# Kernel optimization log

Hardware: AMD Instinct MI355X
Metric: run time of the kernel (lower is better)

Reference implementation:

```python
import jax, jax.numpy as jnp
import numpy as np

T, C, H, S = 2048, 2048, 32, 64
H_KV = 8
L_MAA, L_DEC = 32, 64


def setup_inputs() -> dict:
    key = jax.random.key(0)
    ks = jax.random.split(key, 20)
    def n(k, shp, s=1.0):
        return jax.random.normal(k, shp, dtype=jnp.float32) * s
    sc = 0.02  # init scale for projection weights
    return dict(
        x=n(ks[0], (T, C)),
        state=jnp.zeros((1 + S, C), jnp.float32),
        new_starts=jnp.zeros((T,), bool),
        length=T,
        time_maa_x=n(ks[1], (C,), 0.1),
        time_maa_r=n(ks[2], (C,), 0.1),
        time_maa_k=n(ks[3], (C,), 0.1),
        time_maa_v=n(ks[4], (C,), 0.1),
        time_maa_w=n(ks[5], (C,), 0.1),
        time_maa_g=n(ks[6], (C,), 0.1),
        time_maa_w1=n(ks[7], (C, 5 * L_MAA), sc),
        time_maa_w2=n(ks[8], (5, L_MAA, C), sc),
        time_decay=n(ks[9], (C,), 0.5),
        time_decay_w1=n(ks[10], (C, L_DEC), sc),
        time_decay_w2=n(ks[11], (L_DEC, C), sc),
        Wq=n(ks[12], (C, H * S), sc),
        Wk=n(ks[13], (C, H_KV * S), sc),
        Wv=n(ks[14], (C, H_KV * S), sc),
        Wg=n(ks[15], (C, C), sc),
        Wo=n(ks[16], (C, C), sc),
    )


def reference(x, state, new_starts, length,
              time_maa_x, time_maa_r, time_maa_k, time_maa_v, time_maa_w, time_maa_g,
              time_maa_w1, time_maa_w2,
              time_decay, time_decay_w1, time_decay_w2,
              Wq, Wk, Wv, Wg, Wo):
    # token shift: previous token (state[0] for t=0), zeroed at sequence starts
    sx = jnp.concatenate([state[:1], x[:-1]], axis=0)
    sx = jnp.where(new_starts[:, None], 0.0, sx) - x  # [T, C]

    # data-dependent token-shift mix via LoRA (5 branches: r,k,v,w,g)
    xxx = x + sx * time_maa_x
    m = jnp.tanh(xxx @ time_maa_w1).reshape(T, 5, L_MAA).transpose(1, 0, 2)  # [5,T,L]
    m = jnp.einsum('ntl,nlc->ntc', m, time_maa_w2)  # [5,T,C]
    mr, mk, mv, mw, mg = m
    xr = x + sx * (time_maa_r + mr)
    xk = x + sx * (time_maa_k + mk)
    xv = x + sx * (time_maa_v + mv)
    xw = x + sx * (time_maa_w + mw)
    xg = x + sx * (time_maa_g + mg)

    new_state0 = x[length - 1]  # last valid token

    r = (xr @ Wq).reshape(T, H, S)
    k = (xk @ Wk).reshape(T, H_KV, S)
    v = (xv @ Wv).reshape(T, H_KV, S)

    # per-token decay via LoRA
    dec = time_decay.reshape(1, H, S) + (jnp.tanh(xw @ time_decay_w1) @ time_decay_w2).reshape(T, H, S)
    g = jax.nn.sigmoid(xg @ Wg)  # [T, C]

    reps = H // H_KV
    k = jnp.repeat(k, reps, axis=1)  # [T,H,S]
    v = jnp.repeat(v, reps, axis=1)

    log_w = jnp.maximum(-jnp.exp(dec), -5.0)  # [T,H,S]
    k = k * (1.0 - jnp.exp(log_w))

    s0 = state[1:].reshape(H, S, S)

    def step(s, inp):
        r_t, k_t, v_t, lw_t, ns_t = inp
        s = jnp.where(ns_t, 0.0, s)
        # decay along key dim, then rank-1 update k^T v
        s = s * jnp.exp(lw_t)[:, :, None] + k_t[:, :, None] * v_t[:, None, :]
        o = jnp.einsum('hk,hkv->hv', r_t, s)
        return s, o

    s_fin, out = jax.lax.scan(step, s0, (r, k, v, log_w, new_starts))

    new_state = state.at[0].set(new_state0).at[1:].set(s_fin.reshape(S, H * S))
    y = out.reshape(T, H * S) * g
    return y @ Wo, new_state
```

## Files before the change

### kernel.cpp

```cpp
#include <hip/hip_runtime.h>
#include <hip/hip_bf16.h>
#include <cmath>

#define T_DIM 2048
#define C_DIM 2048
#define NH    32
#define SS    64
#define NC    64
#define CL    32

#define SWZ(r) (((r) + ((r) >> 2)) & 3)

#define WAIT4_BARRIER() do { \
    asm volatile("s_waitcnt vmcnt(4)" ::: "memory"); \
    __builtin_amdgcn_s_barrier(); } while (0)

typedef unsigned short ushort_t;
typedef __attribute__((ext_vector_type(8))) short bf16x8;
typedef __attribute__((ext_vector_type(4))) float f32x4;

__device__ __forceinline__ ushort_t f2bf(float v) {
    union { __hip_bfloat16 b; ushort_t u; } cv;
    cv.b = __float2bfloat16(v);
    return cv.u;
}

__device__ __forceinline__ void gload_lds16(const void* g, void* l) {
    __builtin_amdgcn_global_load_lds((const __attribute__((address_space(1))) void*)g,
                                     (__attribute__((address_space(3))) void*)l,
                                     16, 0, 0);
}

__device__ __forceinline__ float bcast(float x, int k) {
    return __int_as_float(__builtin_amdgcn_readlane(__float_as_int(x), k));
}

__global__ __launch_bounds__(256)
void mega_init(const float* __restrict__ W1, const float* __restrict__ Wd1,
               const float* __restrict__ Wd2, const float* __restrict__ Wq,
               const float* __restrict__ Wk, const float* __restrict__ Wv,
               const float* __restrict__ Wg, const float* __restrict__ W2,
               ushort_t* __restrict__ W1T, ushort_t* __restrict__ Wd1T,
               ushort_t* __restrict__ Wd2T, ushort_t* __restrict__ WqT,
               ushort_t* __restrict__ WkT, ushort_t* __restrict__ WvT,
               ushort_t* __restrict__ WgT, ushort_t* __restrict__ W2Tall,
               const float* __restrict__ x, const float* __restrict__ state,
               const unsigned char* __restrict__ ns, const float* __restrict__ tmx,
               float* __restrict__ sx, ushort_t* __restrict__ xxxb,
               const int* __restrict__ len, float* __restrict__ outstate) {
    __shared__ float t[32][33];
    int bx = blockIdx.x;
    int tid = threadIdx.x;

    if (bx < 4096) {
        int i4 = bx * 256 + tid;
        int idx = i4 * 4;
        int tt = idx >> 11;
        int c = idx & 2047;
        float4 xv = *(const float4*)(x + idx);
        float4 prev;
        if (ns[tt]) prev = make_float4(0.f, 0.f, 0.f, 0.f);
        else if (tt == 0) prev = *(const float4*)(state + c);
        else prev = *(const float4*)(x + idx - C_DIM);
        float4 tm = *(const float4*)(tmx + c);
        float4 s4;
        s4.x = prev.x - xv.x;  s4.y = prev.y - xv.y;
        s4.z = prev.z - xv.z;  s4.w = prev.w - xv.w;
        *(float4*)(sx + idx) = s4;
        ushort4 xb;
        xb.x = f2bf(xv.x + s4.x * tm.x);
        xb.y = f2bf(xv.y + s4.y * tm.y);
        xb.z = f2bf(xv.z + s4.z * tm.z);
        xb.w = f2bf(xv.w + s4.w * tm.w);
        *(ushort4*)(xxxb + idx) = xb;
        return;
    }
    bx -= 4096;
    if (bx < 8) {
        int c = bx * 256 + tid;
        if (c < C_DIM)
            outstate[c] = x[(size_t)(len[0] - 1) * C_DIM + c];
        return;
    }
    bx -= 8;
    const float* W; ushort_t* WT; int K, N, nx;
    if (bx < 512)        {            W = W1;  WT = W1T;  K = 2048; N = 160;  nx = 8;  }
    else if (bx < 768)   { bx -= 512; W = Wd1; WT = Wd1T; K = 2048; N = 64;   nx = 4;  }
    else if (bx < 896)   { bx -= 768; W = Wd2; WT = Wd2T; K = 64;   N = 2048; nx = 64; }
    else if (bx < 4992)  { bx -= 896; W = Wq;  WT = WqT;  K = 2048; N = 2048; nx = 64; }
    else if (bx < 6016)  { bx -= 4992; W = Wk; WT = WkT;  K = 2048; N = 512;  nx = 16; }
    else if (bx < 7040)  { bx -= 6016; W = Wv; WT = WvT;  K = 2048; N = 512;  nx = 16; }
    else if (bx < 11136) { bx -= 7040; W = Wg; WT = WgT;  K = 2048; N = 2048; nx = 64; }
    else {
        bx -= 11136;
        int br = bx >> 6; bx &= 63;
        W = W2 + (size_t)br * 32 * C_DIM; WT = W2Tall + (size_t)br * C_DIM * 32;
        K = 32; N = 2048; nx = 64;
    }
    int n0 = (bx % nx) * 32, k0 = (bx / nx) * 32;
    int tx = tid & 31, ty = tid >> 5;
    #pragma unroll
    for (int i = 0; i < 4; ++i) {
        int k = ty + i * 8;
        float v = 0.f;
        if (n0 + tx < N) v = W[(size_t)(k0 + k) * N + n0 + tx];
        t[k][tx] = v;
    }
    __syncthreads();
    #pragma unroll
    for (int i = 0; i < 4; ++i) {
        int n = ty + i * 8;
        WT[(size_t)(n0 + n) * K + k0 + tx] = f2bf(t[tx][n]);
    }
}

__global__ __launch_bounds__(256)
void w1_splitk(const ushort_t* __restrict__ A,
               const ushort_t* __restrict__ BT,
               float* __restrict__ Wp) {
    const int lda = 2048, K = 2048;
    __shared__ ushort_t As[3][128 * 32];
    __shared__ ushort_t Bs[3][128 * 32];
    int tid = threadIdx.x;
    int wave = tid >> 6, lane = tid & 63;
    int m0 = blockIdx.y * 128, n0 = blockIdx.x * 128;
    int kbase = blockIdx.z * 256;
    float* Cf = Wp + (size_t)blockIdx.z * 2048 * 256;
    int wm = wave >> 1, wn = wave & 1;

    f32x4 acc[4][4] = {};
    int srow0 = wave * 16 + (lane >> 2);
    int schunk = lane & 3;
    int row0 = srow0, row1 = 64 + srow0;
    int gch0 = schunk ^ SWZ(row0), gch1 = schunk ^ SWZ(row1);
    const ushort_t* gA0 = A + (size_t)(m0 + row0) * lda + kbase + gch0 * 8;
    const ushort_t* gA1 = A + (size_t)(m0 + row1) * lda + kbase + gch1 * 8;
    const ushort_t* gB0 = BT + (size_t)(n0 + row0) * K + kbase + gch0 * 8;
    const ushort_t* gB1 = BT + (size_t)(n0 + row1) * K + kbase + gch1 * 8;
    int l0 = row0 * 32 + schunk * 8;
    int l1 = row1 * 32 + schunk * 8;

    const int nt = 8;
    gload_lds16(gA0, &As[0][l0]);
    gload_lds16(gB0, &Bs[0][l0]);
    gload_lds16(gA1, &As[0][l1]);
    gload_lds16(gB1, &Bs[0][l1]);
    gload_lds16(gA0 + 32, &As[1][l0]);
    gload_lds16(gB0 + 32, &Bs[1][l0]);
    gload_lds16(gA1 + 32, &As[1][l1]);
    gload_lds16(gB1 + 32, &Bs[1][l1]);
    WAIT4_BARRIER();

    int fr = lane & 15;
    int fc = lane >> 4;
    int cur = 0;
    for (int t = 0; t < nt; ++t) {
        if (t + 2 < nt) {
            int kk = (t + 2) << 5;
            int nb = cur == 0 ? 2 : cur - 1;
            gload_lds16(gA0 + kk, &As[nb][l0]);
            gload_lds16(gB0 + kk, &Bs[nb][l0]);
            gload_lds16(gA1 + kk, &As[nb][l1]);
            gload_lds16(gB1 + kk, &Bs[nb][l1]);
        }
        bf16x8 af[4], bfr[4];
        #pragma unroll
        for (int mi = 0; mi < 4; ++mi) {
            int r = wm * 64 + mi * 16 + fr;
            af[mi] = *(const bf16x8*)(&As[cur][r * 32 + ((fc ^ SWZ(r)) * 8)]);
        }
        #pragma unroll
        for (int ni = 0; ni < 4; ++ni) {
            int c = wn * 64 + ni * 16 + fr;
            bfr[ni] = *(const bf16x8*)(&Bs[cur][c * 32 + ((fc ^ SWZ(c)) * 8)]);
        }
        #pragma unroll
        for (int mi = 0; mi < 4; ++mi)
            #pragma unroll
            for (int ni = 0; ni < 4; ++ni)
                acc[mi][ni] = __builtin_amdgcn_mfma_f32_16x16x32_bf16(
                    af[mi], bfr[ni], acc[mi][ni], 0, 0, 0);
        WAIT4_BARRIER();
        cur = cur == 2 ? 0 : cur + 1;
    }

    int colin = lane & 15;
    int rquad = lane >> 4;
    #pragma unroll
    for (int mi = 0; mi < 4; ++mi)
        #pragma unroll
        for (int reg = 0; reg < 4; ++reg) {
            int row = m0 + wm * 64 + mi * 16 + rquad * 4 + reg;
            #pragma unroll
            for (int ni = 0; ni < 4; ++ni) {
                int col = n0 + wn * 64 + ni * 16 + colin;
                Cf[(size_t)row * 256 + col] = acc[mi][ni][reg];
            }
        }
}

__global__ __launch_bounds__(256)
void w1_reduce(const float* __restrict__ Wp, ushort_t* __restrict__ mtlb) {
    int idx = (blockIdx.x * 256 + threadIdx.x) * 4;
    float4 s = *(const float4*)(Wp + idx);
    #pragma unroll
    for (int z = 1; z < 8; ++z) {
        float4 p = *(const float4*)(Wp + (size_t)z * 2048 * 256 + idx);
        s.x += p.x; s.y += p.y; s.z += p.z; s.w += p.w;
    }
    ushort4 o;
    o.x = f2bf(tanhf(s.x)); o.y = f2bf(tanhf(s.y));
    o.z = f2bf(tanhf(s.z)); o.w = f2bf(tanhf(s.w));
    *(ushort4*)(mtlb + idx) = o;
}

__global__ __launch_bounds__(256)
void gemm_wo(const ushort_t* __restrict__ A, const ushort_t* __restrict__ BT,
             float* __restrict__ Cf) {
    const int lda = 2048, K = 2048, ldc = 2048;
    __shared__ ushort_t As[3][128 * 32];
    __shared__ ushort_t Bs[3][128 * 32];
    int tid = threadIdx.x;
    int wave = tid >> 6, lane = tid & 63;
    int id = blockIdx.y * 16 + blockIdx.x;
    int xcd = id & 7, j = id >> 3;
    int m0 = ((xcd >> 1) * 4 + (j & 3)) * 128;
    int n0 = ((xcd & 1) * 8 + (j >> 2)) * 128;
    int wm = wave >> 1, wn = wave & 1;

    f32x4 acc[4][4] = {};
    int srow0 = wave * 16 + (lane >> 2);
    int schunk = lane & 3;
    int row0 = srow0, row1 = 64 + srow0;
    int gch0 = schunk ^ SWZ(row0), gch1 = schunk ^ SWZ(row1);
    const ushort_t* gA0 = A + (size_t)(m0 + row0) * lda + gch0 * 8;
    const ushort_t* gA1 = A + (size_t)(m0 + row1) * lda + gch1 * 8;
    const ushort_t* gB0 = BT + (size_t)(n0 + row0) * K + gch0 * 8;
    const ushort_t* gB1 = BT + (size_t)(n0 + row1) * K + gch1 * 8;
    int l0 = row0 * 32 + schunk * 8;
    int l1 = row1 * 32 + schunk * 8;

    const int nt = K >> 5;
    gload_lds16(gA0, &As[0][l0]);
    gload_lds16(gB0, &Bs[0][l0]);
    gload_lds16(gA1, &As[0][l1]);
    gload_lds16(gB1, &Bs[0][l1]);
    gload_lds16(gA0 + 32, &As[1][l0]);
    gload_lds16(gB0 + 32, &Bs[1][l0]);
    gload_lds16(gA1 + 32, &As[1][l1]);
    gload_lds16(gB1 + 32, &Bs[1][l1]);
    WAIT4_BARRIER();

    int fr = lane & 15;
    int fc = lane >> 4;
    int cur = 0;
    for (int t = 0; t < nt; ++t) {
        if (t + 2 < nt) {
            int kk = (t + 2) << 5;
            int nb = cur == 0 ? 2 : cur - 1;
            gload_lds16(gA0 + kk, &As[nb][l0]);
            gload_lds16(gB0 + kk, &Bs[nb][l0]);
            gload_lds16(gA1 + kk, &As[nb][l1]);
            gload_lds16(gB1 + kk, &Bs[nb][l1]);
        }
        bf16x8 af[4], bfr[4];
        #pragma unroll
        for (int mi = 0; mi < 4; ++mi) {
            int r = wm * 64 + mi * 16 + fr;
            af[mi] = *(const bf16x8*)(&As[cur][r * 32 + ((fc ^ SWZ(r)) * 8)]);
        }
        #pragma unroll
        for (int ni = 0; ni < 4; ++ni) {
            int c = wn * 64 + ni * 16 + fr;
            bfr[ni] = *(const bf16x8*)(&Bs[cur][c * 32 + ((fc ^ SWZ(c)) * 8)]);
        }
        #pragma unroll
        for (int mi = 0; mi < 4; ++mi)
            #pragma unroll
            for (int ni = 0; ni < 4; ++ni)
                acc[mi][ni] = __builtin_amdgcn_mfma_f32_16x16x32_bf16(
                    af[mi], bfr[ni], acc[mi][ni], 0, 0, 0);
        WAIT4_BARRIER();
        cur = cur == 2 ? 0 : cur + 1;
    }

    int colin = lane & 15;
    int rquad = lane >> 4;
    #pragma unroll
    for (int mi = 0; mi < 4; ++mi)
        #pragma unroll
        for (int reg = 0; reg < 4; ++reg) {
            int row = m0 + wm * 64 + mi * 16 + rquad * 4 + reg;
            #pragma unroll
            for (int ni = 0; ni < 4; ++ni) {
                int col = n0 + wn * 64 + ni * 16 + colin;
                Cf[(size_t)row * ldc + col] = acc[mi][ni][reg];
            }
        }
}

__global__ __launch_bounds__(256)
void gemm_fused5(const ushort_t* __restrict__ xw, const ushort_t* __restrict__ xk,
                 const ushort_t* __restrict__ xv, const ushort_t* __restrict__ xr,
                 const ushort_t* __restrict__ xg,
                 const ushort_t* __restrict__ Wd1T, const ushort_t* __restrict__ WkT,
                 const ushort_t* __restrict__ WvT, const ushort_t* __restrict__ WqT,
                 const ushort_t* __restrict__ WgT,
                 ushort_t* __restrict__ tw, float* __restrict__ k0g,
                 float* __restrict__ v0g, float* __restrict__ rg,
                 float* __restrict__ gg) {
    const int K = 2048, lda = 2048;
    int id = blockIdx.y * 41 + blockIdx.x;
    int swz = (id & 7) * 82 + (id >> 3);
    int bx = swz >> 4;
    int m0 = (swz & 15) * 128;

    const ushort_t* A; const ushort_t* BT;
    float* Cf = nullptr; ushort_t* Cb = nullptr;
    int ldc, n0, epi;
    if (bx == 0)       { A = xw; BT = Wd1T; Cb = tw;  ldc = 128;  n0 = 0;               epi = 4; }
    else if (bx < 5)   { A = xk; BT = WkT;  Cf = k0g; ldc = 512;  n0 = (bx - 1) * 128;  epi = 0; }
    else if (bx < 9)   { A = xv; BT = WvT;  Cf = v0g; ldc = 512;  n0 = (bx - 5) * 128;  epi = 0; }
    else if (bx < 25)  { A = xr; BT = WqT;  Cf = rg;  ldc = 2048; n0 = (bx - 9) * 128;  epi = 0; }
    else               { A = xg; BT = WgT;  Cf = gg;  ldc = 2048; n0 = (bx - 25) * 128; epi = 2; }

    __shared__ ushort_t As[3][128 * 32];
    __shared__ ushort_t Bs[3][128 * 32];
    int tid = threadIdx.x;
    int wave = tid >> 6, lane = tid & 63;
    int wm = wave >> 1, wn = wave & 1;

    f32x4 acc[4][4] = {};
    int srow0 = wave * 16 + (lane >> 2);
    int schunk = lane & 3;
    int row0 = srow0, row1 = 64 + srow0;
    int gch0 = schunk ^ SWZ(row0), gch1 = schunk ^ SWZ(row1);
    const ushort_t* gA0 = A + (size_t)(m0 + row0) * lda + gch0 * 8;
    const ushort_t* gA1 = A + (size_t)(m0 + row1) * lda + gch1 * 8;
    const ushort_t* gB0 = BT + (size_t)(n0 + row0) * K + gch0 * 8;
    const ushort_t* gB1 = BT + (size_t)(n0 + row1) * K + gch1 * 8;
    int l0 = row0 * 32 + schunk * 8;
    int l1 = row1 * 32 + schunk * 8;

    const int nt = K >> 5;
    gload_lds16(gA0, &As[0][l0]);
    gload_lds16(gB0, &Bs[0][l0]);
    gload_lds16(gA1, &As[0][l1]);
    gload_lds16(gB1, &Bs[0][l1]);
    gload_lds16(gA0 + 32, &As[1][l0]);
    gload_lds16(gB0 + 32, &Bs[1][l0]);
    gload_lds16(gA1 + 32, &As[1][l1]);
    gload_lds16(gB1 + 32, &Bs[1][l1]);
    WAIT4_BARRIER();

    int fr = lane & 15;
    int fc = lane >> 4;
    int cur = 0;
    for (int t = 0; t < nt; ++t) {
        if (t + 2 < nt) {
            int kk = (t + 2) << 5;
            int nb = cur == 0 ? 2 : cur - 1;
            gload_lds16(gA0 + kk, &As[nb][l0]);
            gload_lds16(gB0 + kk, &Bs[nb][l0]);
            gload_lds16(gA1 + kk, &As[nb][l1]);
            gload_lds16(gB1 + kk, &Bs[nb][l1]);
        }
        bf16x8 af[4], bfr[4];
        #pragma unroll
        for (int mi = 0; mi < 4; ++mi) {
            int r = wm * 64 + mi * 16 + fr;
            af[mi] = *(const bf16x8*)(&As[cur][r * 32 + ((fc ^ SWZ(r)) * 8)]);
        }
        #pragma unroll
        for (int ni = 0; ni < 4; ++ni) {
            int c = wn * 64 + ni * 16 + fr;
            bfr[ni] = *(const bf16x8*)(&Bs[cur][c * 32 + ((fc ^ SWZ(c)) * 8)]);
        }
        #pragma unroll
        for (int mi = 0; mi < 4; ++mi)
            #pragma unroll
            for (int ni = 0; ni < 4; ++ni)
                acc[mi][ni] = __builtin_amdgcn_mfma_f32_16x16x32_bf16(
                    af[mi], bfr[ni], acc[mi][ni], 0, 0, 0);
        WAIT4_BARRIER();
        cur = cur == 2 ? 0 : cur + 1;
    }

    int colin = lane & 15;
    int rquad = lane >> 4;
    #pragma unroll
    for (int mi = 0; mi < 4; ++mi) {
        #pragma unroll
        for (int reg = 0; reg < 4; ++reg) {
            int row = m0 + wm * 64 + mi * 16 + rquad * 4 + reg;
            #pragma unroll
            for (int ni = 0; ni < 4; ++ni) {
                int col = n0 + wn * 64 + ni * 16 + colin;
                float v = acc[mi][ni][reg];
                if (epi == 2) v = 1.f / (1.f + __expf(-v));
                else if (epi == 4) v = tanhf(v);
                if (epi == 4) Cb[(size_t)row * ldc + col] = f2bf(v);
                else          Cf[(size_t)row * ldc + col] = v;
            }
        }
    }
}

__global__ __launch_bounds__(256)
void dec_cast(const ushort_t* __restrict__ tw, const ushort_t* __restrict__ Wd2T,
              const float* __restrict__ tdec, float* __restrict__ dec,
              const float* __restrict__ Wo, ushort_t* __restrict__ WoT) {
    int id = blockIdx.x;
    int tid = threadIdx.x;
    if (id >= 256) {
        __shared__ float t[32][33];
        int c = id - 256;
        int n0 = (c & 63) * 32, k0 = (c >> 6) * 32;
        int tx = tid & 31, ty = tid >> 5;
        #pragma unroll
        for (int i = 0; i < 4; ++i) {
            int k = ty + i * 8;
            t[k][tx] = Wo[(size_t)(k0 + k) * 2048 + n0 + tx];
        }
        __syncthreads();
        #pragma unroll
        for (int i = 0; i < 4; ++i) {
            int n = ty + i * 8;
            WoT[(size_t)(n0 + n) * 2048 + k0 + tx] = f2bf(t[tx][n]);
        }
        return;
    }
    const int K = 64, lda = 128, ldc = 2048;
    __shared__ ushort_t As[2][128 * 32];
    __shared__ ushort_t Bs[2][128 * 32];
    int wave = tid >> 6, lane = tid & 63;
    int m0 = (id >> 4) * 128, n0 = (id & 15) * 128;
    int wm = wave >> 1, wn = wave & 1;

    f32x4 acc[4][4] = {};
    int srow0 = wave * 16 + (lane >> 2);
    int schunk = lane & 3;
    int row0 = srow0, row1 = 64 + srow0;
    int gch0 = schunk ^ SWZ(row0), gch1 = schunk ^ SWZ(row1);
    const ushort_t* gA0 = tw + (size_t)(m0 + row0) * lda + gch0 * 8;
    const ushort_t* gA1 = tw + (size_t)(m0 + row1) * lda + gch1 * 8;
    const ushort_t* gB0 = Wd2T + (size_t)(n0 + row0) * K + gch0 * 8;
    const ushort_t* gB1 = Wd2T + (size_t)(n0 + row1) * K + gch1 * 8;
    int l0 = row0 * 32 + schunk * 8;
    int l1 = row1 * 32 + schunk * 8;

    const int nt = K >> 5;
    gload_lds16(gA0, &As[0][l0]);
    gload_lds16(gB0, &Bs[0][l0]);
    gload_lds16(gA1, &As[0][l1]);
    gload_lds16(gB1, &Bs[0][l1]);
    __syncthreads();

    int fr = lane & 15;
    int fc = lane >> 4;
    int cur = 0;
    for (int t = 0; t < nt; ++t) {
        if (t + 1 < nt) {
            int kk = (t + 1) << 5;
            gload_lds16(gA0 + kk, &As[cur ^ 1][l0]);
            gload_lds16(gB0 + kk, &Bs[cur ^ 1][l0]);
            gload_lds16(gA1 + kk, &As[cur ^ 1][l1]);
            gload_lds16(gB1 + kk, &Bs[cur ^ 1][l1]);
        }
        bf16x8 af[4], bfr[4];
        #pragma unroll
        for (int mi = 0; mi < 4; ++mi) {
            int r = wm * 64 + mi * 16 + fr;
            af[mi] = *(const bf16x8*)(&As[cur][r * 32 + ((fc ^ SWZ(r)) * 8)]);
        }
        #pragma unroll
        for (int ni = 0; ni < 4; ++ni) {
            int c = wn * 64 + ni * 16 + fr;
            bfr[ni] = *(const bf16x8*)(&Bs[cur][c * 32 + ((fc ^ SWZ(c)) * 8)]);
        }
        #pragma unroll
        for (int mi = 0; mi < 4; ++mi)
            #pragma unroll
            for (int ni = 0; ni < 4; ++ni)
                acc[mi][ni] = __builtin_amdgcn_mfma_f32_16x16x32_bf16(
                    af[mi], bfr[ni], acc[mi][ni], 0, 0, 0);
        __syncthreads();
        cur ^= 1;
    }

    int colin = lane & 15;
    int rquad = lane >> 4;
    #pragma unroll
    for (int mi = 0; mi < 4; ++mi)
        #pragma unroll
        for (int reg = 0; reg < 4; ++reg) {
            int row = m0 + wm * 64 + mi * 16 + rquad * 4 + reg;
            #pragma unroll
            for (int ni = 0; ni < 4; ++ni) {
                int col = n0 + wn * 64 + ni * 16 + colin;
                dec[(size_t)row * ldc + col] = acc[mi][ni][reg] + tdec[col];
            }
        }
}

__global__ __launch_bounds__(256)
void maa_gemm(const ushort_t* __restrict__ mtlb,
              const ushort_t* __restrict__ W2Tall,
              const float* __restrict__ x, const float* __restrict__ sx,
              const float* __restrict__ tmr, const float* __restrict__ tmk,
              const float* __restrict__ tmv, const float* __restrict__ tmw,
              const float* __restrict__ tmg,
              ushort_t* __restrict__ xr, ushort_t* __restrict__ xk,
              ushort_t* __restrict__ xv, ushort_t* __restrict__ xw,
              ushort_t* __restrict__ xg) {
    int br = blockIdx.z;
    const ushort_t* BT = W2Tall + (size_t)br * C_DIM * 32;
    const float* tm; ushort_t* dst;
    if      (br == 0) { tm = tmr; dst = xr; }
    else if (br == 1) { tm = tmk; dst = xk; }
    else if (br == 2) { tm = tmv; dst = xv; }
    else if (br == 3) { tm = tmw; dst = xw; }
    else              { tm = tmg; dst = xg; }

    __shared__ ushort_t As[128 * 32];
    __shared__ ushort_t Bs[128 * 32];
    int tid = threadIdx.x;
    int wave = tid >> 6, lane = tid & 63;
    int m0 = blockIdx.y * 128, n0 = blockIdx.x * 128;
    int wm = wave >> 1, wn = wave & 1;
    int srow0 = wave * 16 + (lane >> 2);
    int schunk = lane & 3;

    #pragma unroll
    for (int j = 0; j < 2; ++j) {
        int row = j * 64 + srow0;
        int gch = schunk ^ SWZ(row);
        gload_lds16(mtlb + (size_t)(m0 + row) * 256 + br * 32 + gch * 8,
                    As + row * 32 + schunk * 8);
        gload_lds16(BT + (size_t)(n0 + row) * 32 + gch * 8,
                    Bs + row * 32 + schunk * 8);
    }
    __syncthreads();

    int fr = lane & 15;
    int fc = lane >> 4;
    f32x4 acc[4][4] = {};
    bf16x8 af[4], bfr[4];
    #pragma unroll
    for (int mi = 0; mi < 4; ++mi) {
        int r = wm * 64 + mi * 16 + fr;
        af[mi] = *(const bf16x8*)(As + r * 32 + ((fc ^ SWZ(r)) * 8));
    }
    #pragma unroll
    for (int ni = 0; ni < 4; ++ni) {
        int c = wn * 64 + ni * 16 + fr;
        bfr[ni] = *(const bf16x8*)(Bs + c * 32 + ((fc ^ SWZ(c)) * 8));
    }
    #pragma unroll
    for (int mi = 0; mi < 4; ++mi)
        #pragma unroll
        for (int ni = 0; ni < 4; ++ni)
            acc[mi][ni] = __builtin_amdgcn_mfma_f32_16x16x32_bf16(
                af[mi], bfr[ni], acc[mi][ni], 0, 0, 0);

    int colin = lane & 15;
    int rquad = lane >> 4;
    #pragma unroll
    for (int mi = 0; mi < 4; ++mi) {
        #pragma unroll
        for (int reg = 0; reg < 4; ++reg) {
            int row = m0 + wm * 64 + mi * 16 + rquad * 4 + reg;
            #pragma unroll
            for (int ni = 0; ni < 4; ++ni) {
                int col = n0 + wn * 64 + ni * 16 + colin;
                size_t idx = (size_t)row * C_DIM + col;
                float m = acc[mi][ni][reg];
                dst[idx] = f2bf(x[idx] + sx[idx] * (tm[col] + m));
            }
        }
    }
}

__global__ __launch_bounds__(64)
void scan_pass1(const float* __restrict__ k0, const float* __restrict__ v0,
                const float* __restrict__ dec, const unsigned char* __restrict__ ns,
                float* __restrict__ U, float* __restrict__ P) {
    int h = blockIdx.x, c = blockIdx.y, v = threadIdx.x;
    int hk = h >> 2;
    float u[64];
    #pragma unroll
    for (int k = 0; k < 64; ++k) u[k] = 0.f;
    float pk = 1.f;
    int t0 = c * CL;
    float dv_n = dec[(size_t)t0 * 2048 + h * 64 + v];
    float kv_n = k0[(size_t)t0 * 512 + hk * 64 + v];
    float vv_n = v0[(size_t)t0 * 512 + hk * 64 + v];
    unsigned char ns_n = ns[t0];
    for (int i = 0; i < CL; ++i) {
        float dv = dv_n, kv = kv_n, vv = vv_n;
        unsigned char nsv = ns_n;
        if (i + 1 < CL) {
            int t = t0 + i + 1;
            dv_n = dec[(size_t)t * 2048 + h * 64 + v];
            kv_n = k0[(size_t)t * 512 + hk * 64 + v];
            vv_n = v0[(size_t)t * 512 + hk * 64 + v];
            ns_n = ns[t];
        }
        float lw = fmaxf(-__expf(dv), -5.f);
        float ew = __expf(lw);
        float ewp = nsv ? 0.f : ew;
        float kk = kv * (1.f - ew);
        pk *= ewp;
        #pragma unroll
        for (int k = 0; k < 64; ++k) {
            float ewk = bcast(ewp, k);
            float kkk = bcast(kk, k);
            u[k] = fmaf(u[k], ewk, kkk * vv);
        }
    }
    size_t base = ((size_t)h * NC + c) * 4096;
    #pragma unroll
    for (int k = 0; k < 64; ++k) U[base + k * 64 + v] = u[k];
    P[((size_t)h * NC + c) * 64 + v] = pk;
}

__global__ __launch_bounds__(256)
void scan_pass2(float* __restrict__ U, const float* __restrict__ P,
                const float* __restrict__ state, float* __restrict__ outstate) {
    int e = blockIdx.x * 256 + threadIdx.x;
    int h = e >> 12;
    int k = (e >> 6) & 63;
    float s = state[C_DIM + e];
    int rem = e & 4095;
    #pragma unroll 4
    for (int c = 0; c < NC; ++c) {
        size_t ub = ((size_t)h * NC + c) * 4096 + rem;
        float p = P[((size_t)h * NC + c) * 64 + k];
        float u = U[ub];
        U[ub] = s;
        s = fmaf(s, p, u);
    }
    outstate[C_DIM + e] = s;
}

__global__ __launch_bounds__(64)
void scan_pass3(const float* __restrict__ r, const float* __restrict__ k0,
                const float* __restrict__ v0, const float* __restrict__ dec,
                const unsigned char* __restrict__ ns,
                const float* __restrict__ Sstarts, const float* __restrict__ g,
                ushort_t* __restrict__ y0b) {
    int h = blockIdx.x, c = blockIdx.y, v = threadIdx.x;
    int hk = h >> 2;
    float s[64];
    size_t base = ((size_t)h * NC + c) * 4096;
    #pragma unroll
    for (int k = 0; k < 64; ++k) s[k] = Sstarts[base + k * 64 + v];
    int t0 = c * CL;
    float dv_n = dec[(size_t)t0 * 2048 + h * 64 + v];
    float kv_n = k0[(size_t)t0 * 512 + hk * 64 + v];
    float vv_n = v0[(size_t)t0 * 512 + hk * 64 + v];
    float rr_n = r[(size_t)t0 * 2048 + h * 64 + v];
    float gg_n = g[(size_t)t0 * 2048 + h * 64 + v];
    unsigned char ns_n = ns[t0];
    for (int i = 0; i < CL; ++i) {
        float dv = dv_n, kv = kv_n, vv = vv_n, rr = rr_n, gg = gg_n;
        unsigned char nsv = ns_n;
        if (i + 1 < CL) {
            int t = t0 + i + 1;
            dv_n = dec[(size_t)t * 2048 + h * 64 + v];
            kv_n = k0[(size_t)t * 512 + hk * 64 + v];
            vv_n = v0[(size_t)t * 512 + hk * 64 + v];
            rr_n = r[(size_t)t * 2048 + h * 64 + v];
            gg_n = g[(size_t)t * 2048 + h * 64 + v];
            ns_n = ns[t];
        }
        float lw = fmaxf(-__expf(dv), -5.f);
        float ew = __expf(lw);
        float ewl = nsv ? 0.f : ew;
        float kkl = kv * (1.f - ew);
        float o0 = 0.f, o1 = 0.f, o2 = 0.f, o3 = 0.f;
        #pragma unroll
        for (int k = 0; k < 64; k += 4) {
            float s0 = fmaf(s[k],     bcast(ewl, k),     bcast(kkl, k)     * vv); s[k]     = s0; o0 = fmaf(bcast(rr, k),     s0, o0);
            float s1 = fmaf(s[k + 1], bcast(ewl, k + 1), bcast(kkl, k + 1) * vv); s[k + 1] = s1; o1 = fmaf(bcast(rr, k + 1), s1, o1);
            float s2 = fmaf(s[k + 2], bcast(ewl, k + 2), bcast(kkl, k + 2) * vv); s[k + 2] = s2; o2 = fmaf(bcast(rr, k + 2), s2, o2);
            float s3 = fmaf(s[k + 3], bcast(ewl, k + 3), bcast(kkl, k + 3) * vv); s[k + 3] = s3; o3 = fmaf(bcast(rr, k + 3), s3, o3);
        }
        float o = (o0 + o1) + (o2 + o3);
        size_t idx = (size_t)(t0 + i) * 2048 + h * 64 + v;
        y0b[idx] = f2bf(o * gg);
    }
}

extern "C" void kernel_launch(void* const* d_in, const int* in_sizes, int n_in,
                              void* d_out, int out_size, void* d_ws, size_t ws_size,
                              hipStream_t stream) {
    const float* x     = (const float*)d_in[0];
    const float* state = (const float*)d_in[1];
    const unsigned char* ns = (const unsigned char*)d_in[2];
    const int*   len   = (const int*)d_in[3];
    const float* tmx   = (const float*)d_in[4];
    const float* tmr   = (const float*)d_in[5];
    const float* tmk   = (const float*)d_in[6];
    const float* tmv   = (const float*)d_in[7];
    const float* tmw   = (const float*)d_in[8];
    const float* tmg   = (const float*)d_in[9];
    const float* W1    = (const float*)d_in[10];
    const float* W2    = (const float*)d_in[11];
    const float* tdec  = (const float*)d_in[12];
    const float* Wd1   = (const float*)d_in[13];
    const float* Wd2   = (const float*)d_in[14];
    const float* Wq    = (const float*)d_in[15];
    const float* Wk    = (const float*)d_in[16];
    const float* Wv    = (const float*)d_in[17];
    const float* Wg    = (const float*)d_in[18];
    const float* Wo    = (const float*)d_in[19];

    float* out = (float*)d_out;
    float* outstate = out + (size_t)T_DIM * C_DIM;

    char* wsb = (char*)d_ws;
    const size_t MB = 1024 * 1024;
    float*    sx   = (float*)(wsb + 0);
    float*    g    = (float*)(wsb + 0);
    ushort_t* xxxb = (ushort_t*)(wsb + 16 * MB);
    ushort_t* mtlb = (ushort_t*)(wsb + 24 * MB);
    ushort_t* tw   = (ushort_t*)(wsb + 25 * MB);
    float*    P    = (float*)(wsb + 25 * MB + 512 * 1024);
    ushort_t* xr   = (ushort_t*)(wsb + 26 * MB);
    ushort_t* xk   = (ushort_t*)(wsb + 34 * MB);
    float*    dec  = (float*)(wsb + 26 * MB);
    ushort_t* xv   = (ushort_t*)(wsb + 42 * MB);
    ushort_t* WoT  = (ushort_t*)(wsb + 42 * MB);
    ushort_t* xw   = (ushort_t*)(wsb + 50 * MB);
    ushort_t* xg   = (ushort_t*)(wsb + 58 * MB);
    float*    r    = (float*)(wsb + 66 * MB);
    float*    Wp   = (float*)(wsb + 66 * MB);
    float*    k0   = (float*)(wsb + 82 * MB);
    float*    v0   = (float*)(wsb + 86 * MB);
    ushort_t* WqT  = (ushort_t*)(wsb + 90 * MB);
    ushort_t* WkT  = (ushort_t*)(wsb + 98 * MB);
    ushort_t* WvT  = (ushort_t*)(wsb + 100 * MB);
    ushort_t* W1T  = (ushort_t*)(wsb + 102 * MB);
    ushort_t* Wd1T = (ushort_t*)(wsb + 103 * MB);
    ushort_t* Wd2T = (ushort_t*)(wsb + 103 * MB + 512 * 1024);
    ushort_t* W2Tall = (ushort_t*)(wsb + 104 * MB);
    ushort_t* WgT  = (ushort_t*)(wsb + 106 * MB);
    float*    U    = (float*)(wsb + 90 * MB);
    ushort_t* y0b  = xxxb;

    dim3 blk(256);

    mega_init<<<dim3(15560), blk, 0, stream>>>(
        W1, Wd1, Wd2, Wq, Wk, Wv, Wg, W2,
        W1T, Wd1T, Wd2T, WqT, WkT, WvT, WgT, W2Tall,
        x, state, ns, tmx, sx, xxxb, len, outstate);

    w1_splitk<<<dim3(2, 16, 8), blk, 0, stream>>>(xxxb, W1T, Wp);
    w1_reduce<<<dim3(512), blk, 0, stream>>>(Wp, mtlb);
    maa_gemm<<<dim3(16, 16, 5), blk, 0, stream>>>(mtlb, W2Tall, x, sx,
                                                  tmr, tmk, tmv, tmw, tmg,
                                                  xr, xk, xv, xw, xg);
    gemm_fused5<<<dim3(41, 16), blk, 0, stream>>>(xw, xk, xv, xr, xg,
                                                  Wd1T, WkT, WvT, WqT, WgT,
                                                  tw, k0, v0, r, g);
    dec_cast<<<dim3(4352), blk, 0, stream>>>(tw, Wd2T, tdec, dec, Wo, WoT);
    scan_pass1<<<dim3(NH, NC), dim3(64), 0, stream>>>(k0, v0, dec, ns, U, P);
    scan_pass2<<<dim3(512), blk, 0, stream>>>(U, P, state, outstate);
    scan_pass3<<<dim3(NH, NC), dim3(64), 0, stream>>>(r, k0, v0, dec, ns, U, g, y0b);
    gemm_wo<<<dim3(16, 16), blk, 0, stream>>>(y0b, WoT, out);
}
```

Baseline: 441.4 us.

## Split scan state across four waves and split-K the output projection GEMM

```diff
diff --git a/kernel.cpp b/kernel.cpp
--- a/kernel.cpp
+++ b/kernel.cpp
@@ -215,9 +215,9 @@
 }
 
 __global__ __launch_bounds__(256)
-void gemm_wo(const ushort_t* __restrict__ A, const ushort_t* __restrict__ BT,
-             float* __restrict__ Cf) {
-    const int lda = 2048, K = 2048, ldc = 2048;
+void gemm_wo_splitk(const ushort_t* __restrict__ A, const ushort_t* __restrict__ BT,
+                    float* __restrict__ Wp2) {
+    const int lda = 2048, K = 2048;
     __shared__ ushort_t As[3][128 * 32];
     __shared__ ushort_t Bs[3][128 * 32];
     int tid = threadIdx.x;
@@ -226,6 +226,8 @@
     int xcd = id & 7, j = id >> 3;
     int m0 = ((xcd >> 1) * 4 + (j & 3)) * 128;
     int n0 = ((xcd & 1) * 8 + (j >> 2)) * 128;
+    int kbase = blockIdx.z * 1024;
+    float* Cf = Wp2 + (size_t)blockIdx.z * 2048 * 2048;
     int wm = wave >> 1, wn = wave & 1;
 
     f32x4 acc[4][4] = {};
@@ -233,14 +235,14 @@
     int schunk = lane & 3;
     int row0 = srow0, row1 = 64 + srow0;
     int gch0 = schunk ^ SWZ(row0), gch1 = schunk ^ SWZ(row1);
-    const ushort_t* gA0 = A + (size_t)(m0 + row0) * lda + gch0 * 8;
-    const ushort_t* gA1 = A + (size_t)(m0 + row1) * lda + gch1 * 8;
-    const ushort_t* gB0 = BT + (size_t)(n0 + row0) * K + gch0 * 8;
-    const ushort_t* gB1 = BT + (size_t)(n0 + row1) * K + gch1 * 8;
+    const ushort_t* gA0 = A + (size_t)(m0 + row0) * lda + kbase + gch0 * 8;
+    const ushort_t* gA1 = A + (size_t)(m0 + row1) * lda + kbase + gch1 * 8;
+    const ushort_t* gB0 = BT + (size_t)(n0 + row0) * K + kbase + gch0 * 8;
+    const ushort_t* gB1 = BT + (size_t)(n0 + row1) * K + kbase + gch1 * 8;
     int l0 = row0 * 32 + schunk * 8;
     int l1 = row1 * 32 + schunk * 8;
 
-    const int nt = K >> 5;
+    const int nt = 32;
     gload_lds16(gA0, &As[0][l0]);
     gload_lds16(gB0, &Bs[0][l0]);
     gload_lds16(gA1, &As[0][l1]);
@@ -294,9 +296,18 @@
             #pragma unroll
             for (int ni = 0; ni < 4; ++ni) {
                 int col = n0 + wn * 64 + ni * 16 + colin;
-                Cf[(size_t)row * ldc + col] = acc[mi][ni][reg];
+                Cf[(size_t)row * 2048 + col] = acc[mi][ni][reg];
             }
         }
+}
+
+__global__ __launch_bounds__(256)
+void wo_reduce(const float* __restrict__ Wp2, float* __restrict__ out) {
+    int idx = (blockIdx.x * 256 + threadIdx.x) * 4;
+    float4 a = *(const float4*)(Wp2 + idx);
+    float4 b = *(const float4*)(Wp2 + (size_t)2048 * 2048 + idx);
+    a.x += b.x; a.y += b.y; a.z += b.z; a.w += b.w;
+    *(float4*)(out + idx) = a;
 }
 
 __global__ __launch_bounds__(256)
@@ -581,15 +592,18 @@
     }
 }
 
-__global__ __launch_bounds__(64)
+__global__ __launch_bounds__(256)
 void scan_pass1(const float* __restrict__ k0, const float* __restrict__ v0,
                 const float* __restrict__ dec, const unsigned char* __restrict__ ns,
                 float* __restrict__ U, float* __restrict__ P) {
-    int h = blockIdx.x, c = blockIdx.y, v = threadIdx.x;
+    int h = blockIdx.x, c = blockIdx.y;
+    int tid = threadIdx.x;
+    int wave = tid >> 6, v = tid & 63;
     int hk = h >> 2;
-    float u[64];
-    #pragma unroll
-    for (int k = 0; k < 64; ++k) u[k] = 0.f;
+    int kbase = wave * 16;
+    float u[16];
+    #pragma unroll
+    for (int j = 0; j < 16; ++j) u[j] = 0.f;
     float pk = 1.f;
     int t0 = c * CL;
     float dv_n = dec[(size_t)t0 * 2048 + h * 64 + v];
@@ -612,16 +626,15 @@
         float kk = kv * (1.f - ew);
         pk *= ewp;
         #pragma unroll
-        for (int k = 0; k < 64; ++k) {
-            float ewk = bcast(ewp, k);
-            float kkk = bcast(kk, k);
-            u[k] = fmaf(u[k], ewk, kkk * vv);
+        for (int j = 0; j < 16; ++j) {
+            int k = kbase + j;
+            u[j] = fmaf(u[j], bcast(ewp, k), bcast(kk, k) * vv);
         }
     }
     size_t base = ((size_t)h * NC + c) * 4096;
     #pragma unroll
-    for (int k = 0; k < 64; ++k) U[base + k * 64 + v] = u[k];
-    P[((size_t)h * NC + c) * 64 + v] = pk;
+    for (int j = 0; j < 16; ++j) U[base + (kbase + j) * 64 + v] = u[j];
+    if (wave == 0) P[((size_t)h * NC + c) * 64 + v] = pk;
 }
 
 __global__ __launch_bounds__(256)
@@ -643,18 +656,22 @@
     outstate[C_DIM + e] = s;
 }
 
-__global__ __launch_bounds__(64)
+__global__ __launch_bounds__(256)
 void scan_pass3(const float* __restrict__ r, const float* __restrict__ k0,
                 const float* __restrict__ v0, const float* __restrict__ dec,
                 const unsigned char* __restrict__ ns,
                 const float* __restrict__ Sstarts, const float* __restrict__ g,
                 ushort_t* __restrict__ y0b) {
-    int h = blockIdx.x, c = blockIdx.y, v = threadIdx.x;
+    int h = blockIdx.x, c = blockIdx.y;
+    int tid = threadIdx.x;
+    int wave = tid >> 6, v = tid & 63;
     int hk = h >> 2;
-    float s[64];
+    int kbase = wave * 16;
+    __shared__ float osum[2][4][64];
+    float s[16];
     size_t base = ((size_t)h * NC + c) * 4096;
     #pragma unroll
-    for (int k = 0; k < 64; ++k) s[k] = Sstarts[base + k * 64 + v];
+    for (int j = 0; j < 16; ++j) s[j] = Sstarts[base + (kbase + j) * 64 + v];
     int t0 = c * CL;
     float dv_n = dec[(size_t)t0 * 2048 + h * 64 + v];
     float kv_n = k0[(size_t)t0 * 512 + hk * 64 + v];
@@ -678,17 +695,22 @@
         float ew = __expf(lw);
         float ewl = nsv ? 0.f : ew;
         float kkl = kv * (1.f - ew);
-        float o0 = 0.f, o1 = 0.f, o2 = 0.f, o3 = 0.f;
-        #pragma unroll
-        for (int k = 0; k < 64; k += 4) {
-            float s0 = fmaf(s[k],     bcast(ewl, k),     bcast(kkl, k)     * vv); s[k]     = s0; o0 = fmaf(bcast(rr, k),     s0, o0);
-            float s1 = fmaf(s[k + 1], bcast(ewl, k + 1), bcast(kkl, k + 1) * vv); s[k + 1] = s1; o1 = fmaf(bcast(rr, k + 1), s1, o1);
-            float s2 = fmaf(s[k + 2], bcast(ewl, k + 2), bcast(kkl, k + 2) * vv); s[k + 2] = s2; o2 = fmaf(bcast(rr, k + 2), s2, o2);
-            float s3 = fmaf(s[k + 3], bcast(ewl, k + 3), bcast(kkl, k + 3) * vv); s[k + 3] = s3; o3 = fmaf(bcast(rr, k + 3), s3, o3);
-        }
-        float o = (o0 + o1) + (o2 + o3);
-        size_t idx = (size_t)(t0 + i) * 2048 + h * 64 + v;
-        y0b[idx] = f2bf(o * gg);
+        float o0 = 0.f, o1 = 0.f;
+        #pragma unroll
+        for (int j = 0; j < 16; j += 2) {
+            int k = kbase + j;
+            float s0 = fmaf(s[j],     bcast(ewl, k),     bcast(kkl, k)     * vv); s[j]     = s0; o0 = fmaf(bcast(rr, k),     s0, o0);
+            float s1 = fmaf(s[j + 1], bcast(ewl, k + 1), bcast(kkl, k + 1) * vv); s[j + 1] = s1; o1 = fmaf(bcast(rr, k + 1), s1, o1);
+        }
+        osum[i & 1][wave][v] = o0 + o1;
+        asm volatile("s_waitcnt lgkmcnt(0)" ::: "memory");
+        __builtin_amdgcn_s_barrier();
+        if (wave == 0) {
+            float o4 = (osum[i & 1][0][v] + osum[i & 1][1][v])
+                     + (osum[i & 1][2][v] + osum[i & 1][3][v]);
+            size_t idx = (size_t)(t0 + i) * 2048 + h * 64 + v;
+            y0b[idx] = f2bf(o4 * gg);
+        }
     }
 }
 
@@ -747,6 +769,7 @@
     ushort_t* W2Tall = (ushort_t*)(wsb + 104 * MB);
     ushort_t* WgT  = (ushort_t*)(wsb + 106 * MB);
     float*    U    = (float*)(wsb + 90 * MB);
+    float*    Wp2  = (float*)(wsb + 90 * MB);
     ushort_t* y0b  = xxxb;
 
     dim3 blk(256);
@@ -765,8 +788,9 @@
                                                   Wd1T, WkT, WvT, WqT, WgT,
                                                   tw, k0, v0, r, g);
     dec_cast<<<dim3(4352), blk, 0, stream>>>(tw, Wd2T, tdec, dec, Wo, WoT);
-    scan_pass1<<<dim3(NH, NC), dim3(64), 0, stream>>>(k0, v0, dec, ns, U, P);
+    scan_pass1<<<dim3(NH, NC), blk, 0, stream>>>(k0, v0, dec, ns, U, P);
     scan_pass2<<<dim3(512), blk, 0, stream>>>(U, P, state, outstate);
-    scan_pass3<<<dim3(NH, NC), dim3(64), 0, stream>>>(r, k0, v0, dec, ns, U, g, y0b);
-    gemm_wo<<<dim3(16, 16), blk, 0, stream>>>(y0b, WoT, out);
-}
+    scan_pass3<<<dim3(NH, NC), blk, 0, stream>>>(r, k0, v0, dec, ns, U, g, y0b);
+    gemm_wo_splitk<<<dim3(16, 16, 2), blk, 0, stream>>>(y0b, WoT, Wp2);
+    wo_reduce<<<dim3(4096), blk, 0, stream>>>(Wp2, out);
+}
```

Result: slower. 470.0 us (+6.5%).
